# Performance work log

Measured on AMD Instinct MI355X. Metric: run time of the kernel, lower is better.

## Reference

```python
import jax, jax.numpy as jnp
import numpy as np

N, D_IN, D_ATTN, STEPS, TOPK, TAU = 8192, 512, 64, 2, 16, 1.0
LN_EPS = 1e-5


def setup_inputs() -> dict:
    key = jax.random.key(0)
    ks = jax.random.split(key, 6)
    s_in = 1.0 / np.sqrt(D_IN)
    s_at = 1.0 / np.sqrt(D_ATTN)
    return {
        "X": jax.random.normal(ks[0], (N, D_IN), jnp.float32),
        "W1": jax.random.normal(ks[1], (D_ATTN, D_IN), jnp.float32) * s_in,
        "W2": jax.random.normal(ks[2], (D_ATTN, D_ATTN), jnp.float32) * s_at,
        "W3": jax.random.normal(ks[3], (D_ATTN, D_IN), jnp.float32) * s_in,
        "mixW": jax.random.normal(ks[4], (STEPS, D_IN, D_IN), jnp.float32) * s_in,
        "mixB": jax.random.normal(ks[5], (STEPS, D_IN), jnp.float32) * 0.01,
        "gamma": jnp.ones((D_IN,), jnp.float32),
        "beta": jnp.zeros((D_IN,), jnp.float32),
    }


def reference(X, W1, W2, W3, mixW, mixB, gamma, beta):
    # --- adjacency from features (top-k masked attention) ---
    Q = X @ W1.T                    # [N, d_attn]
    K = X @ W3.T                    # [N, d_attn]
    S = (Q @ W2) @ K.T / TAU        # [N, N]  (W2.weight used as raw matrix)
    _, idx = jax.lax.top_k(S, TOPK) # top-k along dim 1, [N, topk]
    mask = jnp.full_like(S, -jnp.inf)
    rows = jnp.arange(N)[:, None]
    mask = mask.at[rows, idx].set(0.0)
    P = jax.nn.softmax(S + mask, axis=1)  # row-sparse (k nonzeros) but dense-stored
    # dropout p=0 (eval mode) -> identity

    # --- iterative message passing with per-step mix ---
    H = X
    Z = jnp.zeros_like(X)
    for n in range(STEPS):  # bidir=False
        H = P @ H
        Z = Z + H @ mixW[n].T + mixB[n]

    # --- residual + LayerNorm ---
    y = X + Z
    mu = jnp.mean(y, axis=-1, keepdims=True)
    var = jnp.mean((y - mu) ** 2, axis=-1, keepdims=True)
    return (y - mu) * jax.lax.rsqrt(var + LN_EPS) * gamma + beta
```

## Files before the change

kernel.cpp:

```cpp
#include <hip/hip_runtime.h>

#define NROWS 8192
#define DIN   512
#define DATT  64
#define KTOP  16
#define CMAX  128
#define SROWS 32
#define NSPLIT 2
#define KSB   256
#define THRC  2.45f
#define NEG_INF (-3.0e38f)

typedef _Float16 f16x8 __attribute__((ext_vector_type(8)));
typedef float    fx4   __attribute__((ext_vector_type(4)));

__global__ void k_conv_f16(const float* __restrict__ in, _Float16* __restrict__ out, int n) {
    int i = blockIdx.x * 256 + threadIdx.x;
    if (i < n) out[i] = (_Float16)in[i];
}

__global__ void k_split(const float* __restrict__ in, _Float16* __restrict__ hi,
                        _Float16* __restrict__ lo, int n) {
    int i = blockIdx.x * 256 + threadIdx.x;
    if (i < n) {
        float x = in[i];
        _Float16 h = (_Float16)x;
        hi[i] = h;
        lo[i] = (_Float16)(x - (float)h);
    }
}

__global__ void k_zero(int* __restrict__ CandCnt) {
    int i = blockIdx.x * 256 + threadIdx.x;
    if (i < NROWS) CandCnt[i] = 0;
}

__global__ void k_wcat(const float* __restrict__ W1, const float* __restrict__ W2,
                       const float* __restrict__ W3, float* __restrict__ Wcat) {
    int id = blockIdx.x * 256 + threadIdx.x;
    int c = id >> 9, k = id & 511;
    float r;
    if (c < 64) {
        float acc = 0.f;
        #pragma unroll 8
        for (int e = 0; e < 64; e++) acc += W1[e*512 + k] * W2[e*64 + c];
        r = acc;
    } else {
        r = W3[(c - 64)*512 + k];
    }
    Wcat[c*512 + k] = r;
}

__launch_bounds__(256)
__global__ void k_proj(const _Float16* __restrict__ Ahi, const _Float16* __restrict__ Alo,
                       const _Float16* __restrict__ Bhi, const _Float16* __restrict__ Blo,
                       float* __restrict__ Cf, _Float16* __restrict__ Ch) {
    const int tid = threadIdx.x, lane = tid & 63, wid = tid >> 6;
    const int bm = blockIdx.x * 128 + wid * 32;
    const int bn = blockIdx.y * 64;
    const int lr = lane & 15, kg = lane >> 4;

    fx4 acc[2][4];
    #pragma unroll
    for (int m = 0; m < 2; m++)
        #pragma unroll
        for (int n = 0; n < 4; n++) acc[m][n] = (fx4){0.f,0.f,0.f,0.f};

    const _Float16* Aph = Ahi + (size_t)(bm + lr) * DIN + kg*8;
    const _Float16* Apl = Alo + (size_t)(bm + lr) * DIN + kg*8;
    const _Float16* Bph = Bhi + (size_t)(bn + lr) * DIN + kg*8;
    const _Float16* Bpl = Blo + (size_t)(bn + lr) * DIN + kg*8;

    for (int k0 = 0; k0 < DIN; k0 += 32) {
        f16x8 ah[2], al[2], bh[4], bl[4];
        #pragma unroll
        for (int m = 0; m < 2; m++) {
            ah[m] = *(const f16x8*)(Aph + (size_t)m*16*DIN + k0);
            al[m] = *(const f16x8*)(Apl + (size_t)m*16*DIN + k0);
        }
        #pragma unroll
        for (int n = 0; n < 4; n++) {
            bh[n] = *(const f16x8*)(Bph + (size_t)n*16*DIN + k0);
            bl[n] = *(const f16x8*)(Bpl + (size_t)n*16*DIN + k0);
        }
        #pragma unroll
        for (int m = 0; m < 2; m++)
            #pragma unroll
            for (int n = 0; n < 4; n++) {
                acc[m][n] = __builtin_amdgcn_mfma_f32_16x16x32_f16(ah[m], bh[n], acc[m][n], 0,0,0);
                acc[m][n] = __builtin_amdgcn_mfma_f32_16x16x32_f16(ah[m], bl[n], acc[m][n], 0,0,0);
                acc[m][n] = __builtin_amdgcn_mfma_f32_16x16x32_f16(al[m], bh[n], acc[m][n], 0,0,0);
            }
    }

    #pragma unroll
    for (int m = 0; m < 2; m++)
        #pragma unroll
        for (int n = 0; n < 4; n++) {
            const int col = bn + n*16 + lr;
            #pragma unroll
            for (int r = 0; r < 4; r++) {
                const int row = bm + m*16 + kg*4 + r;
                const size_t off = (size_t)row * 128 + col;
                float v = acc[m][n][r];
                Cf[off] = v;
                Ch[off] = (_Float16)v;
            }
        }
}

__launch_bounds__(256)
__global__ void k_kstats1(const float* __restrict__ AK, float* __restrict__ KCp,
                          float* __restrict__ ksp) {
    __shared__ float kr[32][64];
    const int tid = threadIdx.x;
    const int r0  = blockIdx.x * 32;
    #pragma unroll
    for (int q = 0; q < 8; q++) {
        int e = tid + q*256;
        int rr = e >> 6, cc = e & 63;
        kr[rr][cc] = AK[(size_t)(r0 + rr) * 128 + 64 + cc];
    }
    __syncthreads();

    const int i0 = tid >> 2;
    const int j0 = (tid & 3) * 16;
    float acc[16];
    #pragma unroll
    for (int e = 0; e < 16; e++) acc[e] = 0.f;
    #pragma unroll 8
    for (int rr = 0; rr < 32; rr++) {
        const float ki = kr[rr][i0];
        #pragma unroll
        for (int e = 0; e < 16; e++) acc[e] += ki * kr[rr][j0 + e];
    }
    float* o = KCp + (size_t)blockIdx.x * 4096 + i0*64 + j0;
    #pragma unroll
    for (int e = 0; e < 16; e++) o[e] = acc[e];

    if (tid < 64) {
        float s = 0.f;
        #pragma unroll 8
        for (int rr = 0; rr < 32; rr++) s += kr[rr][tid];
        ksp[blockIdx.x*64 + tid] = s;
    }
}

__launch_bounds__(256)
__global__ void k_kstats2(const float* __restrict__ KCp, const float* __restrict__ ksp,
                          float* __restrict__ KC, float* __restrict__ ksum) {
    const int o = blockIdx.x*256 + threadIdx.x;
    float s0=0.f, s1=0.f, s2=0.f, s3=0.f;
    for (int b = 0; b < KSB; b += 4) {
        s0 += KCp[(size_t)b*4096 + o];
        s1 += KCp[(size_t)(b+1)*4096 + o];
        s2 += KCp[(size_t)(b+2)*4096 + o];
        s3 += KCp[(size_t)(b+3)*4096 + o];
    }
    KC[o] = (s0+s1) + (s2+s3);
    if (o < 64) {
        float t0=0.f, t1=0.f;
        for (int b = 0; b < KSB; b += 2) {
            t0 += ksp[b*64 + o];
            t1 += ksp[(b+1)*64 + o];
        }
        ksum[o] = t0 + t1;
    }
}

__launch_bounds__(256)
__global__ void k_thr(const float* __restrict__ AK, const float* __restrict__ ksum,
                      const float* __restrict__ KC, float* __restrict__ Thr) {
    __shared__ float sKC[64*65];
    __shared__ float skb[64];
    __shared__ float sa[4][64];
    const int tid = threadIdx.x, lane = tid & 63, wv = tid >> 6;

    for (int e = tid; e < 4096; e += 256)
        sKC[(e >> 6)*65 + (e & 63)] = KC[e];
    if (tid < 64) skb[tid] = ksum[tid] * (1.f/(float)NROWS);
    sa[wv][lane] = AK[(size_t)(blockIdx.x*4 + wv) * 128 + lane];
    __syncthreads();

    const int row = blockIdx.x*4 + wv;
    const float a_l = sa[wv][lane];
    float w = 0.f;
    #pragma unroll 16
    for (int d = 0; d < 64; d++) w += sKC[lane*65 + d] * sa[wv][d];
    float p  = a_l * w;
    float mu = a_l * skb[lane];
    #pragma unroll
    for (int off = 1; off < 64; off <<= 1) {
        p  += __shfl_xor(p,  off);
        mu += __shfl_xor(mu, off);
    }
    if (lane == 0) {
        float var = p * (1.f/(float)NROWS) - mu*mu;
        Thr[row] = mu + THRC * sqrtf(fmaxf(var, 0.f));
    }
}

__launch_bounds__(256)
__global__ void k_sfilter(const _Float16* __restrict__ AKh, const float* __restrict__ Thr,
                          int* __restrict__ CandIdx, int* __restrict__ CandCnt) {
    const int tid = threadIdx.x, lane = tid & 63, wid = tid >> 6;
    const int bm = blockIdx.x * SROWS;
    const int lr = lane & 15, kg = lane >> 4;

    __shared__ int scnt[SROWS];
    __shared__ int sbase[SROWS];
    __shared__ int scand[SROWS][CMAX];
    if (tid < SROWS) scnt[tid] = 0;

    f16x8 af[2][2];
    #pragma unroll
    for (int m = 0; m < 2; m++)
        #pragma unroll
        for (int ks = 0; ks < 2; ks++)
            af[m][ks] = *(const f16x8*)(AKh + (size_t)(bm + m*16 + lr)*128 + ks*32 + kg*8);

    float thr[2][4];
    #pragma unroll
    for (int m = 0; m < 2; m++)
        #pragma unroll
        for (int r = 0; r < 4; r++)
            thr[m][r] = Thr[bm + m*16 + kg*4 + r];

    __syncthreads();

    const int c0 = blockIdx.y * (NROWS/NSPLIT) + wid*64;
    f16x8 bf[4][2], bnx[4][2];
    #pragma unroll
    for (int n = 0; n < 4; n++)
        #pragma unroll
        for (int ks = 0; ks < 2; ks++)
            bnx[n][ks] = *(const f16x8*)(AKh + (size_t)(c0 + n*16 + lr)*128 + 64 + ks*32 + kg*8);

    const int NIT = (NROWS/NSPLIT)/256;
    for (int it = 0; it < NIT; ++it) {
        #pragma unroll
        for (int n = 0; n < 4; n++)
            #pragma unroll
            for (int ks = 0; ks < 2; ks++)
                bf[n][ks] = bnx[n][ks];
        const int cbase = c0 + it*256;
        if (it + 1 < NIT) {
            const int cnx = cbase + 256;
            #pragma unroll
            for (int n = 0; n < 4; n++)
                #pragma unroll
                for (int ks = 0; ks < 2; ks++)
                    bnx[n][ks] = *(const f16x8*)(AKh + (size_t)(cnx + n*16 + lr)*128 + 64 + ks*32 + kg*8);
        }

        fx4 acc[2][4];
        #pragma unroll
        for (int m = 0; m < 2; m++)
            #pragma unroll
            for (int n = 0; n < 4; n++) acc[m][n] = (fx4){0.f,0.f,0.f,0.f};
        #pragma unroll
        for (int ks = 0; ks < 2; ks++)
            #pragma unroll
            for (int m = 0; m < 2; m++)
                #pragma unroll
                for (int n = 0; n < 4; n++)
                    acc[m][n] = __builtin_amdgcn_mfma_f32_16x16x32_f16(af[m][ks], bf[n][ks], acc[m][n], 0,0,0);

        #pragma unroll
        for (int m = 0; m < 2; m++) {
            #pragma unroll
            for (int r = 0; r < 4; r++) {
                const int row = m*16 + kg*4 + r;
                const float t = thr[m][r];
                #pragma unroll
                for (int n = 0; n < 4; n++) {
                    const float v = acc[m][n][r];
                    if (v > t) {
                        const int p = atomicAdd(&scnt[row], 1);
                        if (p < CMAX) scand[row][p] = cbase + n*16 + lr;
                    }
                }
            }
        }
    }

    __syncthreads();
    if (tid < SROWS) sbase[tid] = atomicAdd(&CandCnt[bm + tid], min(scnt[tid], CMAX));
    __syncthreads();
    for (int e = tid; e < SROWS*CMAX; e += 256) {
        const int row = e / CMAX, slot = e % CMAX;
        if (slot < min(scnt[row], CMAX)) {
            const int dst = sbase[row] + slot;
            if (dst < CMAX) CandIdx[(size_t)(bm + row)*CMAX + dst] = scand[row][slot];
        }
    }
}

__launch_bounds__(256)
__global__ void k_sel(const float* __restrict__ AK, const int* __restrict__ CandIdx,
                      const int* __restrict__ CandCnt,
                      float* __restrict__ Pval, int* __restrict__ Pidx) {
    const int wv   = threadIdx.x >> 6;
    const int row  = blockIdx.x*4 + wv;
    const int lane = threadIdx.x & 63;
    const int cnt  = min(CandCnt[row], CMAX);

    __shared__ float ss[4][CMAX];
    __shared__ int   sx[4][CMAX];

    const fx4* a4 = (const fx4*)(AK + (size_t)row * 128);

    float sv[2]; int si[2];
    #pragma unroll
    for (int q = 0; q < 2; q++) {
        const int c = lane + q*64;
        if (c < cnt) {
            const int idx = CandIdx[(size_t)row * CMAX + c];
            const fx4* k4 = (const fx4*)(AK + (size_t)idx * 128 + 64);
            float p0 = 0.f, p1 = 0.f, p2 = 0.f, p3 = 0.f;
            #pragma unroll
            for (int d = 0; d < 4; d++) {
                fx4 a0 = a4[d*4+0], k0 = k4[d*4+0];
                fx4 a1 = a4[d*4+1], k1 = k4[d*4+1];
                fx4 a2 = a4[d*4+2], k2 = k4[d*4+2];
                fx4 a3 = a4[d*4+3], k3 = k4[d*4+3];
                p0 += a0[0]*k0[0] + a0[1]*k0[1] + a0[2]*k0[2] + a0[3]*k0[3];
                p1 += a1[0]*k1[0] + a1[1]*k1[1] + a1[2]*k1[2] + a1[3]*k1[3];
                p2 += a2[0]*k2[0] + a2[1]*k2[1] + a2[2]*k2[2] + a2[3]*k2[3];
                p3 += a3[0]*k3[0] + a3[1]*k3[1] + a3[2]*k3[2] + a3[3]*k3[3];
            }
            sv[q] = (p0 + p1) + (p2 + p3); si[q] = idx;
        } else { sv[q] = NEG_INF; si[q] = 0x7fffffff; }
        ss[wv][c] = sv[q];
        sx[wv][c] = si[q];
    }

    float m = fmaxf(sv[0], sv[1]);
    #pragma unroll
    for (int off = 1; off < 64; off <<= 1) m = fmaxf(m, __shfl_xor(m, off));

    int r0 = 0, r1 = 0;
    #pragma unroll 4
    for (int j = 0; j < cnt; j++) {
        const float sj = ss[wv][j];
        const int   ij = sx[wv][j];
        r0 += (sj > sv[0]) || (sj == sv[0] && ij < si[0]);
        r1 += (sj > sv[1]) || (sj == sv[1] && ij < si[1]);
    }

    const float e0 = (lane      < cnt && r0 < KTOP) ? __expf(sv[0] - m) : 0.f;
    const float e1 = (lane + 64 < cnt && r1 < KTOP) ? __expf(sv[1] - m) : 0.f;
    float Z = e0 + e1;
    #pragma unroll
    for (int off = 1; off < 64; off <<= 1) Z += __shfl_xor(Z, off);
    const float rZ = 1.f / Z;

    if (lane < cnt && r0 < KTOP) {
        Pval[(size_t)row*KTOP + r0] = e0 * rZ;
        Pidx[(size_t)row*KTOP + r0] = si[0];
    }
    if (lane + 64 < cnt && r1 < KTOP) {
        Pval[(size_t)row*KTOP + r1] = e1 * rZ;
        Pidx[(size_t)row*KTOP + r1] = si[1];
    }
    if (lane >= cnt && lane < KTOP) {
        Pval[(size_t)row*KTOP + lane] = 0.f;
        Pidx[(size_t)row*KTOP + lane] = row;
    }
}

__launch_bounds__(256)
__global__ void k_gather(const float* __restrict__ Pval, const int* __restrict__ Pidx,
                         const _Float16* __restrict__ Hin, _Float16* __restrict__ Hout) {
    const int wv = threadIdx.x >> 6, lane = threadIdx.x & 63;
    const int row = blockIdx.x*4 + wv;
    const float pvl = Pval[row*KTOP + (lane & 15)];
    const int   pil = Pidx[row*KTOP + (lane & 15)];

    float acc[8];
    #pragma unroll
    for (int j = 0; j < 8; j++) acc[j] = 0.f;
    #pragma unroll
    for (int t = 0; t < KTOP; t++) {
        const float p  = __shfl(pvl, t);
        const int   ix = __shfl(pil, t);
        f16x8 h = *(const f16x8*)(Hin + (size_t)ix*DIN + lane*8);
        #pragma unroll
        for (int j = 0; j < 8; j++) acc[j] += p * (float)h[j];
    }
    f16x8 o;
    #pragma unroll
    for (int j = 0; j < 8; j++) o[j] = (_Float16)acc[j];
    *(f16x8*)(Hout + (size_t)row*DIN + lane*8) = o;
}

template<int RM, int RN, int WR, int WC, bool ACCUM>
__launch_bounds__(256)
__global__ void k_gemm_nt(const _Float16* __restrict__ A, const _Float16* __restrict__ B,
                          float* __restrict__ Cf, const float* __restrict__ bias,
                          int M, int N, int K) {
    const int tid  = threadIdx.x;
    const int lane = tid & 63;
    const int wid  = tid >> 6;
    const int wr   = wid / WC;
    const int wc   = wid % WC;
    const int bm   = blockIdx.x * (WR*RM*16) + wr*(RM*16);
    const int bn   = blockIdx.y * (WC*RN*16) + wc*(RN*16);
    const int lr   = lane & 15;
    const int kg   = lane >> 4;

    fx4 acc[RM][RN];
    #pragma unroll
    for (int m = 0; m < RM; m++)
        #pragma unroll
        for (int n = 0; n < RN; n++)
            acc[m][n] = (fx4){0.f, 0.f, 0.f, 0.f};

    const _Float16* Ap = A + (size_t)(bm + lr) * K + kg*8;
    const _Float16* Bp = B + (size_t)(bn + lr) * K + kg*8;

    for (int k0 = 0; k0 < K; k0 += 32) {
        f16x8 af[RM], bf[RN];
        #pragma unroll
        for (int m = 0; m < RM; m++)
            af[m] = *(const f16x8*)(Ap + (size_t)m*16*K + k0);
        #pragma unroll
        for (int n = 0; n < RN; n++)
            bf[n] = *(const f16x8*)(Bp + (size_t)n*16*K + k0);
        #pragma unroll
        for (int m = 0; m < RM; m++)
            #pragma unroll
            for (int n = 0; n < RN; n++)
                acc[m][n] = __builtin_amdgcn_mfma_f32_16x16x32_f16(af[m], bf[n], acc[m][n], 0, 0, 0);
    }

    #pragma unroll
    for (int m = 0; m < RM; m++) {
        #pragma unroll
        for (int n = 0; n < RN; n++) {
            const int col = bn + n*16 + lr;
            const float bv = bias[col];
            #pragma unroll
            for (int r = 0; r < 4; r++) {
                const int row = bm + m*16 + kg*4 + r;
                const size_t off = (size_t)row * N + col;
                float v = acc[m][n][r] + bv;
                if (ACCUM) v += Cf[off];
                Cf[off] = v;
            }
        }
    }
}

__launch_bounds__(256)
__global__ void k_ln(const float* __restrict__ X, const float* __restrict__ Z,
                     const float* __restrict__ gamma, const float* __restrict__ beta,
                     float* __restrict__ out) {
    const int row = blockIdx.x, tid = threadIdx.x;
    const size_t base = (size_t)row * DIN;
    float y0 = X[base + tid]       + Z[base + tid];
    float y1 = X[base + tid + 256] + Z[base + tid + 256];
    float s  = y0 + y1;
    float s2 = y0*y0 + y1*y1;
    #pragma unroll
    for (int off = 32; off > 0; off >>= 1) {
        s  += __shfl_down(s,  off);
        s2 += __shfl_down(s2, off);
    }
    __shared__ float as_[4], as2_[4], mv[2];
    const int lane = tid & 63, w = tid >> 6;
    if (lane == 0) { as_[w] = s; as2_[w] = s2; }
    __syncthreads();
    if (tid == 0) {
        float ts = as_[0] + as_[1] + as_[2] + as_[3];
        float t2 = as2_[0] + as2_[1] + as2_[2] + as2_[3];
        float mu  = ts / 512.f;
        float var = t2 / 512.f - mu*mu;
        mv[0] = mu; mv[1] = rsqrtf(var + 1e-5f);
    }
    __syncthreads();
    const float mu = mv[0], rs = mv[1];
    out[base + tid]       = (y0 - mu) * rs * gamma[tid]       + beta[tid];
    out[base + tid + 256] = (y1 - mu) * rs * gamma[tid + 256] + beta[tid + 256];
}

extern "C" void kernel_launch(void* const* d_in, const int* in_sizes, int n_in,
                              void* d_out, int out_size, void* d_ws, size_t ws_size,
                              hipStream_t stream) {
    const float* X     = (const float*)d_in[0];
    const float* W1    = (const float*)d_in[1];
    const float* W2    = (const float*)d_in[2];
    const float* W3    = (const float*)d_in[3];
    const float* mixW  = (const float*)d_in[4];
    const float* mixB  = (const float*)d_in[5];
    const float* gamma = (const float*)d_in[6];
    const float* beta  = (const float*)d_in[7];
    float* out = (float*)d_out;

    char* ws = (char*)d_ws;
    size_t off = 0;
    auto alloc = [&](size_t bytes) {
        void* p = ws + off;
        off += (bytes + 255) & ~(size_t)255;
        return p;
    };
    _Float16* Xhi  = (_Float16*)alloc((size_t)NROWS*DIN*2);
    _Float16* Xlo  = (_Float16*)alloc((size_t)NROWS*DIN*2);
    float*    Wcat = (float*)alloc((size_t)128*DIN*4);
    _Float16* Whi  = (_Float16*)alloc((size_t)128*DIN*2);
    _Float16* Wlo  = (_Float16*)alloc((size_t)128*DIN*2);
    float*    Af32 = (float*)alloc((size_t)NROWS*128*4);
    _Float16* AKh  = (_Float16*)alloc((size_t)NROWS*128*2);
    _Float16* mWh  = (_Float16*)alloc((size_t)2*DIN*DIN*2);
    float*    KCp  = (float*)alloc((size_t)KSB*4096*4);
    float*    ksp  = (float*)alloc((size_t)KSB*64*4);
    float*    ksum = (float*)alloc(64*4);
    float*    KC   = (float*)alloc(4096*4);
    float*    Thr  = (float*)alloc((size_t)NROWS*4);
    float*    Pval = (float*)alloc((size_t)NROWS*KTOP*4);
    int*      Pidx = (int*)alloc((size_t)NROWS*KTOP*4);
    int*      CandIdx = (int*)alloc((size_t)NROWS*CMAX*4);
    int*      CandCnt = (int*)alloc((size_t)NROWS*4);
    _Float16* H1h  = (_Float16*)alloc((size_t)NROWS*DIN*2);
    _Float16* H2h  = (_Float16*)alloc((size_t)NROWS*DIN*2);
    float*    Zacc = (float*)alloc((size_t)NROWS*DIN*4);
    (void)ws_size; (void)in_sizes; (void)n_in; (void)out_size;

    dim3 b256(256);

    k_zero<<<dim3(NROWS/256), b256, 0, stream>>>(CandCnt);
    k_split<<<dim3(NROWS*DIN/256), b256, 0, stream>>>(X, Xhi, Xlo, NROWS*DIN);
    k_wcat<<<dim3(128*DIN/256), b256, 0, stream>>>(W1, W2, W3, Wcat);
    k_split<<<dim3(128*DIN/256), b256, 0, stream>>>(Wcat, Whi, Wlo, 128*DIN);
    k_conv_f16<<<dim3(2*DIN*DIN/256), b256, 0, stream>>>(mixW, mWh, 2*DIN*DIN);

    k_proj<<<dim3(NROWS/128, 2), b256, 0, stream>>>(Xhi, Xlo, Whi, Wlo, Af32, AKh);

    k_kstats1<<<dim3(KSB), b256, 0, stream>>>(Af32, KCp, ksp);
    k_kstats2<<<dim3(16), b256, 0, stream>>>(KCp, ksp, KC, ksum);
    k_thr<<<dim3(NROWS/4), b256, 0, stream>>>(Af32, ksum, KC, Thr);

    k_sfilter<<<dim3(NROWS/SROWS, NSPLIT), b256, 0, stream>>>(AKh, Thr, CandIdx, CandCnt);

    k_sel<<<dim3(NROWS/4), b256, 0, stream>>>(Af32, CandIdx, CandCnt, Pval, Pidx);

    k_gather<<<dim3(NROWS/4), b256, 0, stream>>>(Pval, Pidx, Xhi, H1h);
    k_gemm_nt<4,4,2,2,false><<<dim3(NROWS/128, DIN/128), b256, 0, stream>>>(
        H1h, mWh, Zacc, mixB, NROWS, DIN, DIN);
    k_gather<<<dim3(NROWS/4), b256, 0, stream>>>(Pval, Pidx, H1h, H2h);
    k_gemm_nt<4,4,2,2,true><<<dim3(NROWS/128, DIN/128), b256, 0, stream>>>(
        H2h, mWh + (size_t)DIN*DIN, Zacc, mixB + DIN, NROWS, DIN, DIN);
    k_ln<<<dim3(NROWS), b256, 0, stream>>>(X, Zacc, gamma, beta, out);
}
```

Measured before the change: 305.4 us.

## Stage mix GEMM tiles through LDS, fuse weight prep kernels, batch threshold rows

Replaces the register-direct mix GEMM with an LDS-staged version that uses global_load_lds direct copies into a swizzled shared tile, a 128x64 block tile and a K step of 64. It also merges the zeroing, Wcat and weight-split kernels into one, and has each wave in the threshold kernel handle four rows using shuffles instead of a shared staging array. The aim is to cut redundant global loads in the GEMM and launch overhead in the prologue. In exchange the GEMM adds two barriers per K step and gets no double buffering.

```diff
diff --git a/kernel.cpp b/kernel.cpp
--- a/kernel.cpp
+++ b/kernel.cpp
@@ -14,6 +14,11 @@
 typedef _Float16 f16x8 __attribute__((ext_vector_type(8)));
 typedef float    fx4   __attribute__((ext_vector_type(4)));
 
+__device__ __forceinline__ void gload_lds16(const void* g, void* l) {
+    __builtin_amdgcn_global_load_lds((const __attribute__((address_space(1))) void*)g,
+                                     (__attribute__((address_space(3))) void*)l, 16, 0, 0);
+}
+
 __global__ void k_conv_f16(const float* __restrict__ in, _Float16* __restrict__ out, int n) {
     int i = blockIdx.x * 256 + threadIdx.x;
     if (i < n) out[i] = (_Float16)in[i];
@@ -30,14 +35,11 @@
     }
 }
 
-__global__ void k_zero(int* __restrict__ CandCnt) {
-    int i = blockIdx.x * 256 + threadIdx.x;
-    if (i < NROWS) CandCnt[i] = 0;
-}
-
-__global__ void k_wcat(const float* __restrict__ W1, const float* __restrict__ W2,
-                       const float* __restrict__ W3, float* __restrict__ Wcat) {
+__global__ void k_wsplit(const float* __restrict__ W1, const float* __restrict__ W2,
+                         const float* __restrict__ W3, _Float16* __restrict__ Whi,
+                         _Float16* __restrict__ Wlo, int* __restrict__ CandCnt) {
     int id = blockIdx.x * 256 + threadIdx.x;
+    if (id < NROWS) CandCnt[id] = 0;
     int c = id >> 9, k = id & 511;
     float r;
     if (c < 64) {
@@ -48,7 +50,9 @@
     } else {
         r = W3[(c - 64)*512 + k];
     }
-    Wcat[c*512 + k] = r;
+    _Float16 h = (_Float16)r;
+    Whi[id] = h;
+    Wlo[id] = (_Float16)(r - (float)h);
 }
 
 __launch_bounds__(256)
@@ -173,30 +177,31 @@
                       const float* __restrict__ KC, float* __restrict__ Thr) {
     __shared__ float sKC[64*65];
     __shared__ float skb[64];
-    __shared__ float sa[4][64];
     const int tid = threadIdx.x, lane = tid & 63, wv = tid >> 6;
 
     for (int e = tid; e < 4096; e += 256)
         sKC[(e >> 6)*65 + (e & 63)] = KC[e];
     if (tid < 64) skb[tid] = ksum[tid] * (1.f/(float)NROWS);
-    sa[wv][lane] = AK[(size_t)(blockIdx.x*4 + wv) * 128 + lane];
-    __syncthreads();
-
-    const int row = blockIdx.x*4 + wv;
-    const float a_l = sa[wv][lane];
-    float w = 0.f;
-    #pragma unroll 16
-    for (int d = 0; d < 64; d++) w += sKC[lane*65 + d] * sa[wv][d];
-    float p  = a_l * w;
-    float mu = a_l * skb[lane];
-    #pragma unroll
-    for (int off = 1; off < 64; off <<= 1) {
-        p  += __shfl_xor(p,  off);
-        mu += __shfl_xor(mu, off);
-    }
-    if (lane == 0) {
-        float var = p * (1.f/(float)NROWS) - mu*mu;
-        Thr[row] = mu + THRC * sqrtf(fmaxf(var, 0.f));
+    __syncthreads();
+
+    #pragma unroll
+    for (int j = 0; j < 4; j++) {
+        const int row = blockIdx.x*16 + wv*4 + j;
+        const float a_l = AK[(size_t)row * 128 + lane];
+        float w = 0.f;
+        #pragma unroll 16
+        for (int d = 0; d < 64; d++) w += sKC[lane*65 + d] * __shfl(a_l, d);
+        float p  = a_l * w;
+        float mu = a_l * skb[lane];
+        #pragma unroll
+        for (int off = 1; off < 64; off <<= 1) {
+            p  += __shfl_xor(p,  off);
+            mu += __shfl_xor(mu, off);
+        }
+        if (lane == 0) {
+            float var = p * (1.f/(float)NROWS) - mu*mu;
+            Thr[row] = mu + THRC * sqrtf(fmaxf(var, 0.f));
+        }
     }
 }
 
@@ -394,55 +399,75 @@
     *(f16x8*)(Hout + (size_t)row*DIN + lane*8) = o;
 }
 
-template<int RM, int RN, int WR, int WC, bool ACCUM>
-__launch_bounds__(256)
-__global__ void k_gemm_nt(const _Float16* __restrict__ A, const _Float16* __restrict__ B,
-                          float* __restrict__ Cf, const float* __restrict__ bias,
-                          int M, int N, int K) {
-    const int tid  = threadIdx.x;
-    const int lane = tid & 63;
-    const int wid  = tid >> 6;
-    const int wr   = wid / WC;
-    const int wc   = wid % WC;
-    const int bm   = blockIdx.x * (WR*RM*16) + wr*(RM*16);
-    const int bn   = blockIdx.y * (WC*RN*16) + wc*(RN*16);
-    const int lr   = lane & 15;
-    const int kg   = lane >> 4;
-
-    fx4 acc[RM][RN];
-    #pragma unroll
-    for (int m = 0; m < RM; m++)
-        #pragma unroll
-        for (int n = 0; n < RN; n++)
-            acc[m][n] = (fx4){0.f, 0.f, 0.f, 0.f};
-
-    const _Float16* Ap = A + (size_t)(bm + lr) * K + kg*8;
-    const _Float16* Bp = B + (size_t)(bn + lr) * K + kg*8;
-
-    for (int k0 = 0; k0 < K; k0 += 32) {
-        f16x8 af[RM], bf[RN];
-        #pragma unroll
-        for (int m = 0; m < RM; m++)
-            af[m] = *(const f16x8*)(Ap + (size_t)m*16*K + k0);
-        #pragma unroll
-        for (int n = 0; n < RN; n++)
-            bf[n] = *(const f16x8*)(Bp + (size_t)n*16*K + k0);
-        #pragma unroll
-        for (int m = 0; m < RM; m++)
-            #pragma unroll
-            for (int n = 0; n < RN; n++)
-                acc[m][n] = __builtin_amdgcn_mfma_f32_16x16x32_f16(af[m], bf[n], acc[m][n], 0, 0, 0);
-    }
-
-    #pragma unroll
-    for (int m = 0; m < RM; m++) {
-        #pragma unroll
-        for (int n = 0; n < RN; n++) {
+template<bool ACCUM>
+__launch_bounds__(256)
+__global__ void k_gemm_lds(const _Float16* __restrict__ A, const _Float16* __restrict__ B,
+                           float* __restrict__ Cf, const float* __restrict__ bias,
+                           int M, int N, int K) {
+    __shared__ __align__(16) char smem[24576];
+    const int tid = threadIdx.x, lane = tid & 63, wid = tid >> 6;
+    const int bm = blockIdx.x * 128;
+    const int bn = blockIdx.y * 64;
+    const int lr = lane & 15, kg = lane >> 4;
+
+    const int srow  = lane >> 3;
+    const int scolh = ((lane & 7) ^ srow) * 8;
+
+    fx4 acc[2][4];
+    #pragma unroll
+    for (int m = 0; m < 2; m++)
+        #pragma unroll
+        for (int n = 0; n < 4; n++) acc[m][n] = (fx4){0.f,0.f,0.f,0.f};
+
+    const int sw = (lr & 7) << 4;
+
+    for (int k0 = 0; k0 < K; k0 += 64) {
+        #pragma unroll
+        for (int q = 0; q < 4; q++) {
+            const int r = (wid*4 + q)*8 + srow;
+            gload_lds16(A + (size_t)(bm + r)*K + k0 + scolh, smem + (wid*4 + q)*1024);
+        }
+        #pragma unroll
+        for (int q = 0; q < 2; q++) {
+            const int r = (wid*2 + q)*8 + srow;
+            gload_lds16(B + (size_t)(bn + r)*K + k0 + scolh, smem + 16384 + (wid*2 + q)*1024);
+        }
+        __syncthreads();
+
+        f16x8 af[2][2], bf[4][2];
+        #pragma unroll
+        for (int m = 0; m < 2; m++) {
+            const int arow = wid*32 + m*16 + lr;
+            #pragma unroll
+            for (int ks = 0; ks < 2; ks++)
+                af[m][ks] = *(const f16x8*)(smem + arow*128 + ((ks*64 + kg*16) ^ sw));
+        }
+        #pragma unroll
+        for (int n = 0; n < 4; n++) {
+            const int brow = n*16 + lr;
+            #pragma unroll
+            for (int ks = 0; ks < 2; ks++)
+                bf[n][ks] = *(const f16x8*)(smem + 16384 + brow*128 + ((ks*64 + kg*16) ^ sw));
+        }
+        #pragma unroll
+        for (int ks = 0; ks < 2; ks++)
+            #pragma unroll
+            for (int m = 0; m < 2; m++)
+                #pragma unroll
+                for (int n = 0; n < 4; n++)
+                    acc[m][n] = __builtin_amdgcn_mfma_f32_16x16x32_f16(af[m][ks], bf[n][ks], acc[m][n], 0,0,0);
+        __syncthreads();
+    }
+
+    #pragma unroll
+    for (int m = 0; m < 2; m++) {
+        #pragma unroll
+        for (int n = 0; n < 4; n++) {
             const int col = bn + n*16 + lr;
             const float bv = bias[col];
             #pragma unroll
             for (int r = 0; r < 4; r++) {
-                const int row = bm + m*16 + kg*4 + r;
+                const int row = bm + wid*32 + m*16 + kg*4 + r;
                 const size_t off = (size_t)row * N + col;
                 float v = acc[m][n][r] + bv;
                 if (ACCUM) v += Cf[off];
@@ -506,7 +531,6 @@
     };
     _Float16* Xhi  = (_Float16*)alloc((size_t)NROWS*DIN*2);
     _Float16* Xlo  = (_Float16*)alloc((size_t)NROWS*DIN*2);
-    float*    Wcat = (float*)alloc((size_t)128*DIN*4);
     _Float16* Whi  = (_Float16*)alloc((size_t)128*DIN*2);
     _Float16* Wlo  = (_Float16*)alloc((size_t)128*DIN*2);
     float*    Af32 = (float*)alloc((size_t)NROWS*128*4);
@@ -528,27 +552,25 @@
 
     dim3 b256(256);
 
-    k_zero<<<dim3(NROWS/256), b256, 0, stream>>>(CandCnt);
+    k_wsplit<<<dim3(128*DIN/256), b256, 0, stream>>>(W1, W2, W3, Whi, Wlo, CandCnt);
     k_split<<<dim3(NROWS*DIN/256), b256, 0, stream>>>(X, Xhi, Xlo, NROWS*DIN);
-    k_wcat<<<dim3(128*DIN/256), b256, 0, stream>>>(W1, W2, W3, Wcat);
-    k_split<<<dim3(128*DIN/256), b256, 0, stream>>>(Wcat, Whi, Wlo, 128*DIN);
     k_conv_f16<<<dim3(2*DIN*DIN/256), b256, 0, stream>>>(mixW, mWh, 2*DIN*DIN);
 
     k_proj<<<dim3(NROWS/128, 2), b256, 0, stream>>>(Xhi, Xlo, Whi, Wlo, Af32, AKh);
 
     k_kstats1<<<dim3(KSB), b256, 0, stream>>>(Af32, KCp, ksp);
     k_kstats2<<<dim3(16), b256, 0, stream>>>(KCp, ksp, KC, ksum);
-    k_thr<<<dim3(NROWS/4), b256, 0, stream>>>(Af32, ksum, KC, Thr);
+    k_thr<<<dim3(NROWS/16), b256, 0, stream>>>(Af32, ksum, KC, Thr);
 
     k_sfilter<<<dim3(NROWS/SROWS, NSPLIT), b256, 0, stream>>>(AKh, Thr, CandIdx, CandCnt);
 
     k_sel<<<dim3(NROWS/4), b256, 0, stream>>>(Af32, CandIdx, CandCnt, Pval, Pidx);
 
     k_gather<<<dim3(NROWS/4), b256, 0, stream>>>(Pval, Pidx, Xhi, H1h);
-    k_gemm_nt<4,4,2,2,false><<<dim3(NROWS/128, DIN/128), b256, 0, stream>>>(
+    k_gemm_lds<false><<<dim3(NROWS/128, DIN/64), b256, 0, stream>>>(
         H1h, mWh, Zacc, mixB, NROWS, DIN, DIN);
     k_gather<<<dim3(NROWS/4), b256, 0, stream>>>(Pval, Pidx, H1h, H2h);
-    k_gemm_nt<4,4,2,2,true><<<dim3(NROWS/128, DIN/128), b256, 0, stream>>>(
+    k_gemm_lds<true><<<dim3(NROWS/128, DIN/64), b256, 0, stream>>>(
         H2h, mWh + (size_t)DIN*DIN, Zacc, mixB + DIN, NROWS, DIN, DIN);
     k_ln<<<dim3(NROWS), b256, 0, stream>>>(X, Zacc, gamma, beta, out);
 }
```

Measured after the change: 285.8 us. 6.4% less time.
